# Kernel tuning notes

Measured on AMD Instinct MI355X. Metric: run time of the kernel, lower is better.

## Reference

```python
import jax, jax.numpy as jnp
import numpy as np

N_NODES = 20000
N_EDGES = 640000
IN_DIM = 128
HID = 128
OUT_DIM = 3
N_GRAPHS = 32


def setup_inputs() -> dict:
    key = jax.random.key(0)
    ks = jax.random.split(key, 12)
    x = jax.random.normal(ks[0], (N_NODES, IN_DIM), dtype=jnp.float32)
    edge_index = jax.random.randint(ks[1], (2, N_EDGES), 0, N_NODES, dtype=jnp.int64)
    batch = jnp.sort(jax.random.randint(ks[2], (N_NODES,), 0, N_GRAPHS, dtype=jnp.int64))
    batch = batch.at[0].set(0).at[-1].set(N_GRAPHS - 1)
    s = 0.05
    W_gcn = jax.random.normal(ks[3], (IN_DIM, HID), jnp.float32) * s
    b_gcn = jnp.zeros((HID,), jnp.float32)
    W_sage_l = jax.random.normal(ks[4], (HID, HID), jnp.float32) * s  # neighbor branch
    W_sage_r = jax.random.normal(ks[5], (HID, HID), jnp.float32) * s  # root branch
    b_sage = jnp.zeros((HID,), jnp.float32)
    W_fc1 = jax.random.normal(ks[6], (HID, HID), jnp.float32) * s
    b_fc1 = jnp.zeros((HID,), jnp.float32)
    W_fc2 = jax.random.normal(ks[7], (HID, OUT_DIM), jnp.float32) * s
    b_fc2 = jnp.zeros((OUT_DIM,), jnp.float32)
    return {
        'x': x, 'edge_index': edge_index, 'batch': batch,
        'W_gcn': W_gcn, 'b_gcn': b_gcn,
        'W_sage_l': W_sage_l, 'W_sage_r': W_sage_r, 'b_sage': b_sage,
        'W_fc1': W_fc1, 'b_fc1': b_fc1, 'W_fc2': W_fc2, 'b_fc2': b_fc2,
    }


def reference(x, edge_index, batch, W_gcn, b_gcn, W_sage_l, W_sage_r, b_sage,
              W_fc1, b_fc1, W_fc2, b_fc2):
    n = x.shape[0]
    row, col = edge_index[0], edge_index[1]  # source -> target

    # ---- GCNConv: symmetric-normalized aggregation with self-loops ----
    h = x @ W_gcn  # [N, H]
    loops = jnp.arange(n, dtype=row.dtype)
    row_sl = jnp.concatenate([row, loops])
    col_sl = jnp.concatenate([col, loops])
    deg = jax.ops.segment_sum(jnp.ones_like(col_sl, dtype=h.dtype), col_sl,
                              num_segments=n)
    dinv = jnp.where(deg > 0, jax.lax.rsqrt(deg), 0.0)
    norm = dinv[row_sl] * dinv[col_sl]  # [E+N]
    h_gcn = jax.ops.segment_sum(h[row_sl] * norm[:, None], col_sl,
                                num_segments=n) + b_gcn
    h_gcn = jax.nn.relu(h_gcn)

    # ---- SAGEConv (mean aggregator) ----
    cnt = jax.ops.segment_sum(jnp.ones_like(col, dtype=h_gcn.dtype), col,
                              num_segments=n)
    neigh = jax.ops.segment_sum(h_gcn[row], col, num_segments=n)
    neigh = neigh / jnp.maximum(cnt, 1.0)[:, None]
    h_sage = neigh @ W_sage_l + h_gcn @ W_sage_r + b_sage
    h_sage = jax.nn.relu(h_sage)

    # ---- global_add_pool (num_graphs = 32 < 50) ----
    pooled = jax.ops.segment_sum(h_sage, batch, num_segments=N_GRAPHS)  # [G, H]

    # ---- MLP head ----
    out = jax.nn.relu(pooled @ W_fc1 + b_fc1) @ W_fc2 + b_fc2  # [G, 3]
    return out
```

## Files before the change

kernel.cpp:

```cpp
#include <hip/hip_runtime.h>

#define N_NODES 20000
#define N_EDGES 640000
#define HID 128
#define N_GRAPHS 32

__global__ __launch_bounds__(256) void hist_k(const int* __restrict__ col,
                                              int* __restrict__ cnt) {
    int e = blockIdx.x * blockDim.x + threadIdx.x;
    if (e < N_EDGES) {
        int c = col[e];
        if ((unsigned)c < N_NODES) atomicAdd(&cnt[c], 1);
    }
}

__global__ __launch_bounds__(1024) void scan_k(const int* __restrict__ cnt,
                                               int* __restrict__ offs,
                                               int* __restrict__ cursor,
                                               float* __restrict__ dinv) {
    __shared__ int sums[1024];
    const int t = threadIdx.x;
    const int CHUNK = 20;
    int base = t * CHUNK;
    int s = 0;
    for (int j = 0; j < CHUNK; ++j) {
        int i = base + j;
        if (i < N_NODES) s += cnt[i];
    }
    sums[t] = s;
    __syncthreads();
    for (int off = 1; off < 1024; off <<= 1) {
        int v = sums[t];
        int add = (t >= off) ? sums[t - off] : 0;
        __syncthreads();
        sums[t] = v + add;
        __syncthreads();
    }
    int run = (t > 0) ? sums[t - 1] : 0;
    for (int j = 0; j < CHUNK; ++j) {
        int i = base + j;
        if (i < N_NODES) {
            offs[i] = run;
            cursor[i] = run;
            int c = cnt[i];
            run += c;
            dinv[i] = rsqrtf((float)(c + 1));
        }
    }
    if (t == 1023) offs[N_NODES] = run;
}

__global__ __launch_bounds__(256) void fill_k(const int* __restrict__ row,
                                              const int* __restrict__ col,
                                              int* __restrict__ cursor,
                                              int* __restrict__ csr_src,
                                              float* __restrict__ csr_norm,
                                              const float* __restrict__ dinv) {
    int e = blockIdx.x * blockDim.x + threadIdx.x;
    if (e < N_EDGES) {
        int c = col[e];
        int r = row[e];
        if ((unsigned)c < N_NODES && (unsigned)r < N_NODES) {
            int p = atomicAdd(&cursor[c], 1);
            csr_src[p] = r;
            csr_norm[p] = dinv[r];
        }
    }
}

__global__ __launch_bounds__(256) void gemm128_k(const float* __restrict__ X,
                                                 const float* __restrict__ W,
                                                 float* __restrict__ Y,
                                                 int nrows) {
    __shared__ float ws[128 * 128];
    __shared__ float xs[32 * 128];
    const int t = threadIdx.x;
    for (int i = t; i < 4096; i += 256)
        ((float4*)ws)[i] = ((const float4*)W)[i];
    const int rg = t >> 5;
    const int c4 = (t & 31) * 4;
    const int ntiles = (nrows + 31) / 32;
    for (int tile = blockIdx.x; tile < ntiles; tile += gridDim.x) {
        const int row0 = tile * 32;
        __syncthreads();
#pragma unroll
        for (int i = 0; i < 4; ++i) {
            int idx = t + i * 256;
            int rr = row0 + (idx >> 5);
            float4 v = (rr < nrows) ? ((const float4*)X)[(size_t)rr * 32 + (idx & 31)]
                                    : make_float4(0.f, 0.f, 0.f, 0.f);
            ((float4*)xs)[idx] = v;
        }
        __syncthreads();
        float4 acc[4];
        acc[0] = acc[1] = acc[2] = acc[3] = make_float4(0.f, 0.f, 0.f, 0.f);
#pragma unroll 4
        for (int k = 0; k < 128; k += 2) {
            float4 w0 = *(const float4*)&ws[(k + 0) * 128 + c4];
            float4 w1 = *(const float4*)&ws[(k + 1) * 128 + c4];
#pragma unroll
            for (int i = 0; i < 4; ++i) {
                float2 xv = *(const float2*)&xs[(rg * 4 + i) * 128 + k];
                acc[i].x = fmaf(xv.x, w0.x, fmaf(xv.y, w1.x, acc[i].x));
                acc[i].y = fmaf(xv.x, w0.y, fmaf(xv.y, w1.y, acc[i].y));
                acc[i].z = fmaf(xv.x, w0.z, fmaf(xv.y, w1.z, acc[i].z));
                acc[i].w = fmaf(xv.x, w0.w, fmaf(xv.y, w1.w, acc[i].w));
            }
        }
#pragma unroll
        for (int i = 0; i < 4; ++i) {
            int rr = row0 + rg * 4 + i;
            if (rr < nrows) *(float4*)&Y[(size_t)rr * 128 + c4] = acc[i];
        }
    }
}

__global__ __launch_bounds__(256) void gcn_agg_k(const float* __restrict__ h,
                                                 const int* __restrict__ offs,
                                                 const int* __restrict__ src,
                                                 const float* __restrict__ nrm,
                                                 const float* __restrict__ dinv,
                                                 const float* __restrict__ bias,
                                                 float* __restrict__ out) {
    const int wave = threadIdx.x >> 6;
    const int lane = threadIdx.x & 63;
    const int half = lane >> 5;
    const int node = (blockIdx.x * 4 + wave) * 2 + half;
    const int c4 = (lane & 31) * 4;
    const int nd = (node < N_NODES) ? node : (N_NODES - 1);
    const float dc = dinv[nd];
    float4 hv = *(const float4*)&h[(size_t)nd * 128 + c4];
    float4 acc = make_float4(dc * hv.x, dc * hv.y, dc * hv.z, dc * hv.w);
    const int beg = offs[nd];
    const int deg = offs[nd + 1] - beg;
    const int mdeg = max(deg, __shfl(deg, lane ^ 32));
    for (int j = 0; j < mdeg; j += 4) {
        int i0 = (j + 0 < deg) ? beg + j + 0 : 0;
        int i1 = (j + 1 < deg) ? beg + j + 1 : 0;
        int i2 = (j + 2 < deg) ? beg + j + 2 : 0;
        int i3 = (j + 3 < deg) ? beg + j + 3 : 0;
        float w0 = (j + 0 < deg) ? nrm[i0] : 0.f;
        float w1 = (j + 1 < deg) ? nrm[i1] : 0.f;
        float w2 = (j + 2 < deg) ? nrm[i2] : 0.f;
        float w3 = (j + 3 < deg) ? nrm[i3] : 0.f;
        int s0 = src[i0], s1 = src[i1], s2 = src[i2], s3 = src[i3];
        float4 v0 = *(const float4*)&h[(size_t)s0 * 128 + c4];
        float4 v1 = *(const float4*)&h[(size_t)s1 * 128 + c4];
        float4 v2 = *(const float4*)&h[(size_t)s2 * 128 + c4];
        float4 v3 = *(const float4*)&h[(size_t)s3 * 128 + c4];
        acc.x = fmaf(w0, v0.x, fmaf(w1, v1.x, fmaf(w2, v2.x, fmaf(w3, v3.x, acc.x))));
        acc.y = fmaf(w0, v0.y, fmaf(w1, v1.y, fmaf(w2, v2.y, fmaf(w3, v3.y, acc.y))));
        acc.z = fmaf(w0, v0.z, fmaf(w1, v1.z, fmaf(w2, v2.z, fmaf(w3, v3.z, acc.z))));
        acc.w = fmaf(w0, v0.w, fmaf(w1, v1.w, fmaf(w2, v2.w, fmaf(w3, v3.w, acc.w))));
    }
    float4 b = *(const float4*)&bias[c4];
    float4 o;
    o.x = fmaxf(fmaf(dc, acc.x, b.x), 0.f);
    o.y = fmaxf(fmaf(dc, acc.y, b.y), 0.f);
    o.z = fmaxf(fmaf(dc, acc.z, b.z), 0.f);
    o.w = fmaxf(fmaf(dc, acc.w, b.w), 0.f);
    if (node < N_NODES) *(float4*)&out[(size_t)node * 128 + c4] = o;
}

__global__ __launch_bounds__(256) void sage_agg_k(const float* __restrict__ hg,
                                                  const int* __restrict__ offs,
                                                  const int* __restrict__ src,
                                                  float* __restrict__ out) {
    const int wave = threadIdx.x >> 6;
    const int lane = threadIdx.x & 63;
    const int half = lane >> 5;
    const int node = (blockIdx.x * 4 + wave) * 2 + half;
    const int c4 = (lane & 31) * 4;
    const int nd = (node < N_NODES) ? node : (N_NODES - 1);
    float4 acc = make_float4(0.f, 0.f, 0.f, 0.f);
    const int beg = offs[nd];
    const int deg = offs[nd + 1] - beg;
    const int mdeg = max(deg, __shfl(deg, lane ^ 32));
    for (int j = 0; j < mdeg; j += 4) {
        int i0 = (j + 0 < deg) ? beg + j + 0 : 0;
        int i1 = (j + 1 < deg) ? beg + j + 1 : 0;
        int i2 = (j + 2 < deg) ? beg + j + 2 : 0;
        int i3 = (j + 3 < deg) ? beg + j + 3 : 0;
        float w0 = (j + 0 < deg) ? 1.f : 0.f;
        float w1 = (j + 1 < deg) ? 1.f : 0.f;
        float w2 = (j + 2 < deg) ? 1.f : 0.f;
        float w3 = (j + 3 < deg) ? 1.f : 0.f;
        int s0 = src[i0], s1 = src[i1], s2 = src[i2], s3 = src[i3];
        float4 v0 = *(const float4*)&hg[(size_t)s0 * 128 + c4];
        float4 v1 = *(const float4*)&hg[(size_t)s1 * 128 + c4];
        float4 v2 = *(const float4*)&hg[(size_t)s2 * 128 + c4];
        float4 v3 = *(const float4*)&hg[(size_t)s3 * 128 + c4];
        acc.x = fmaf(w0, v0.x, fmaf(w1, v1.x, fmaf(w2, v2.x, fmaf(w3, v3.x, acc.x))));
        acc.y = fmaf(w0, v0.y, fmaf(w1, v1.y, fmaf(w2, v2.y, fmaf(w3, v3.y, acc.y))));
        acc.z = fmaf(w0, v0.z, fmaf(w1, v1.z, fmaf(w2, v2.z, fmaf(w3, v3.z, acc.z))));
        acc.w = fmaf(w0, v0.w, fmaf(w1, v1.w, fmaf(w2, v2.w, fmaf(w3, v3.w, acc.w))));
    }
    float inv = 1.0f / (float)max(deg, 1);
    float4 o;
    o.x = acc.x * inv;
    o.y = acc.y * inv;
    o.z = acc.z * inv;
    o.w = acc.w * inv;
    if (node < N_NODES) *(float4*)&out[(size_t)node * 128 + c4] = o;
}

__global__ __launch_bounds__(256) void combine_k(const float* __restrict__ An,
                                                 const float* __restrict__ Bh,
                                                 const float* __restrict__ Wl,
                                                 const float* __restrict__ Wr,
                                                 const float* __restrict__ bias,
                                                 float* __restrict__ Y) {
    __shared__ float ws[128 * 128];
    __shared__ float xs[32 * 128];
    const int t = threadIdx.x;
    const int rg = t >> 5;
    const int c4 = (t & 31) * 4;
    const int ntiles = (N_NODES + 31) / 32;
    for (int tile = blockIdx.x; tile < ntiles; tile += gridDim.x) {
        const int row0 = tile * 32;
        float4 acc[4];
        {
            float4 b = *(const float4*)&bias[c4];
            acc[0] = acc[1] = acc[2] = acc[3] = b;
        }
#pragma unroll
        for (int m = 0; m < 2; ++m) {
            const float* Wm = m ? Wr : Wl;
            const float* Xm = m ? Bh : An;
            __syncthreads();
            for (int i = t; i < 4096; i += 256)
                ((float4*)ws)[i] = ((const float4*)Wm)[i];
#pragma unroll
            for (int i = 0; i < 4; ++i) {
                int idx = t + i * 256;
                int rr = row0 + (idx >> 5);
                float4 v = (rr < N_NODES) ? ((const float4*)Xm)[(size_t)rr * 32 + (idx & 31)]
                                          : make_float4(0.f, 0.f, 0.f, 0.f);
                ((float4*)xs)[idx] = v;
            }
            __syncthreads();
#pragma unroll 4
            for (int k = 0; k < 128; k += 2) {
                float4 w0 = *(const float4*)&ws[(k + 0) * 128 + c4];
                float4 w1 = *(const float4*)&ws[(k + 1) * 128 + c4];
#pragma unroll
                for (int i = 0; i < 4; ++i) {
                    float2 xv = *(const float2*)&xs[(rg * 4 + i) * 128 + k];
                    acc[i].x = fmaf(xv.x, w0.x, fmaf(xv.y, w1.x, acc[i].x));
                    acc[i].y = fmaf(xv.x, w0.y, fmaf(xv.y, w1.y, acc[i].y));
                    acc[i].z = fmaf(xv.x, w0.z, fmaf(xv.y, w1.z, acc[i].z));
                    acc[i].w = fmaf(xv.x, w0.w, fmaf(xv.y, w1.w, acc[i].w));
                }
            }
        }
#pragma unroll
        for (int i = 0; i < 4; ++i) {
            int rr = row0 + rg * 4 + i;
            if (rr < N_NODES) {
                float4 o = acc[i];
                o.x = fmaxf(o.x, 0.f);
                o.y = fmaxf(o.y, 0.f);
                o.z = fmaxf(o.z, 0.f);
                o.w = fmaxf(o.w, 0.f);
                *(float4*)&Y[(size_t)rr * 128 + c4] = o;
            }
        }
    }
}

#define POOL_ROWS 64
__global__ __launch_bounds__(256) void pool_k(const float* __restrict__ H,
                                              const int* __restrict__ batch,
                                              float* __restrict__ pooled) {
    const int r0 = blockIdx.x * POOL_ROWS;
    const int t = threadIdx.x;
    const int d = t & 127, half = t >> 7;
    const int rend = min(r0 + POOL_ROWS, N_NODES);
    int i = r0 + half;
    if (i >= rend) return;
    int cur = batch[i];
    float acc = 0.f;
    for (; i < rend; i += 2) {
        int g = batch[i];
        if (g != cur) {
            atomicAdd(&pooled[cur * 128 + d], acc);
            acc = 0.f;
            cur = g;
        }
        acc += H[(size_t)i * 128 + d];
    }
    atomicAdd(&pooled[cur * 128 + d], acc);
}

__global__ __launch_bounds__(128) void head_k(const float* __restrict__ pooled,
                                              const float* __restrict__ Wfc1,
                                              const float* __restrict__ bfc1,
                                              const float* __restrict__ Wfc2,
                                              const float* __restrict__ bfc2,
                                              float* __restrict__ out) {
    __shared__ float pl[128];
    __shared__ float tmp[128];
    const int g = blockIdx.x;
    const int t = threadIdx.x;
    pl[t] = pooled[g * 128 + t];
    __syncthreads();
    float a = bfc1[t];
#pragma unroll 8
    for (int k = 0; k < 128; ++k) a = fmaf(pl[k], Wfc1[k * 128 + t], a);
    tmp[t] = fmaxf(a, 0.f);
    __syncthreads();
    if (t < 3) {
        float a2 = bfc2[t];
        for (int k = 0; k < 128; ++k) a2 = fmaf(tmp[k], Wfc2[k * 3 + t], a2);
        out[g * 3 + t] = a2;
    }
}

extern "C" void kernel_launch(void* const* d_in, const int* in_sizes, int n_in,
                              void* d_out, int out_size, void* d_ws, size_t ws_size,
                              hipStream_t stream) {
    const float* x      = (const float*)d_in[0];
    const int*   ei     = (const int*)d_in[1];
    const int*   batch  = (const int*)d_in[2];
    const float* W_gcn  = (const float*)d_in[3];
    const float* b_gcn  = (const float*)d_in[4];
    const float* W_sl   = (const float*)d_in[5];
    const float* W_sr   = (const float*)d_in[6];
    const float* b_sage = (const float*)d_in[7];
    const float* W_fc1  = (const float*)d_in[8];
    const float* b_fc1  = (const float*)d_in[9];
    const float* W_fc2  = (const float*)d_in[10];
    const float* b_fc2  = (const float*)d_in[11];
    float* out = (float*)d_out;

    char* base = (char*)d_ws;
    size_t off = 0;
    auto take = [&](size_t bytes) -> void* {
        void* p = base + off;
        off += (bytes + 255) & ~(size_t)255;
        return p;
    };
    int*   cnt      = (int*)take((size_t)N_NODES * 4);
    int*   offs     = (int*)take((size_t)(N_NODES + 1) * 4);
    int*   cursor   = (int*)take((size_t)N_NODES * 4);
    float* dinv     = (float*)take((size_t)N_NODES * 4);
    int*   csr_src  = (int*)take((size_t)N_EDGES * 4);
    float* csr_norm = (float*)take((size_t)N_EDGES * 4);
    float* bufA     = (float*)take((size_t)N_NODES * HID * 4);
    float* bufB     = (float*)take((size_t)N_NODES * HID * 4);
    float* pooled   = (float*)take((size_t)N_GRAPHS * HID * 4);

    const int* row = ei;
    const int* col = ei + N_EDGES;

    hipMemsetAsync(cnt, 0, (size_t)N_NODES * 4, stream);
    hipMemsetAsync(pooled, 0, (size_t)N_GRAPHS * HID * 4, stream);

    hist_k<<<(N_EDGES + 255) / 256, 256, 0, stream>>>(col, cnt);
    scan_k<<<1, 1024, 0, stream>>>(cnt, offs, cursor, dinv);
    fill_k<<<(N_EDGES + 255) / 256, 256, 0, stream>>>(row, col, cursor, csr_src, csr_norm, dinv);

    const int ntiles = (N_NODES + 31) / 32;
    const int agg_blocks = (N_NODES + 7) / 8;
    gemm128_k<<<ntiles, 256, 0, stream>>>(x, W_gcn, bufA, N_NODES);
    gcn_agg_k<<<agg_blocks, 256, 0, stream>>>(bufA, offs, csr_src, csr_norm,
                                              dinv, b_gcn, bufB);
    sage_agg_k<<<agg_blocks, 256, 0, stream>>>(bufB, offs, csr_src, bufA);
    combine_k<<<ntiles, 256, 0, stream>>>(bufA, bufB, W_sl, W_sr, b_sage, bufA);
    pool_k<<<(N_NODES + POOL_ROWS - 1) / POOL_ROWS, 256, 0, stream>>>(bufA, batch, pooled);
    head_k<<<N_GRAPHS, 128, 0, stream>>>(pooled, W_fc1, b_fc1, W_fc2, b_fc2, out);
}
```

Baseline: 351.1 us.

## Split single-block prefix scan into multi-block reduce-then-scan kernels

Replaces the single 1024-thread block scan over node degrees with two kernels: one computes per-block sums with wavefront shuffles, the second does a block-local scan and adds a serially computed block prefix. The aim is to spread the scan across many CUs instead of one, so the strided serial chunk loops and their uncoalesced loads go away. It adds an extra kernel launch and a serial loop over up to 79 block sums per block.

```diff
diff --git a/kernel.cpp b/kernel.cpp
--- a/kernel.cpp
+++ b/kernel.cpp
@@ -4,6 +4,9 @@
 #define N_EDGES 640000
 #define HID 128
 #define N_GRAPHS 32
+
+#define SCAN_BLK 256
+#define SCAN_NBLK ((N_NODES + SCAN_BLK - 1) / SCAN_BLK)
 
 __global__ __launch_bounds__(256) void hist_k(const int* __restrict__ col,
                                               int* __restrict__ cnt) {
@@ -14,40 +17,54 @@
     }
 }
 
-__global__ __launch_bounds__(1024) void scan_k(const int* __restrict__ cnt,
-                                               int* __restrict__ offs,
-                                               int* __restrict__ cursor,
-                                               float* __restrict__ dinv) {
-    __shared__ int sums[1024];
-    const int t = threadIdx.x;
-    const int CHUNK = 20;
-    int base = t * CHUNK;
-    int s = 0;
-    for (int j = 0; j < CHUNK; ++j) {
-        int i = base + j;
-        if (i < N_NODES) s += cnt[i];
-    }
-    sums[t] = s;
+__global__ __launch_bounds__(SCAN_BLK) void scanA_k(const int* __restrict__ cnt,
+                                                    int* __restrict__ blkSum) {
+    __shared__ int wsum[SCAN_BLK / 64];
+    const int b = blockIdx.x, t = threadIdx.x;
+    const int i = b * SCAN_BLK + t;
+    int v = (i < N_NODES) ? cnt[i] : 0;
+#pragma unroll
+    for (int o = 1; o < 64; o <<= 1) v += __shfl_xor(v, o);
+    if ((t & 63) == 0) wsum[t >> 6] = v;
     __syncthreads();
-    for (int off = 1; off < 1024; off <<= 1) {
-        int v = sums[t];
-        int add = (t >= off) ? sums[t - off] : 0;
+    if (t == 0) {
+        int s = 0;
+#pragma unroll
+        for (int w = 0; w < SCAN_BLK / 64; ++w) s += wsum[w];
+        blkSum[b] = s;
+    }
+}
+
+__global__ __launch_bounds__(SCAN_BLK) void scanB_k(const int* __restrict__ cnt,
+                                                    const int* __restrict__ blkSum,
+                                                    int* __restrict__ offs,
+                                                    int* __restrict__ cursor,
+                                                    float* __restrict__ dinv) {
+    __shared__ int sm[SCAN_BLK];
+    __shared__ int base_s;
+    const int b = blockIdx.x, t = threadIdx.x;
+    const int i = b * SCAN_BLK + t;
+    const int v = (i < N_NODES) ? cnt[i] : 0;
+    sm[t] = v;
+    if (t == 0) {
+        int s = 0;
+        for (int k = 0; k < b; ++k) s += blkSum[k];
+        base_s = s;
+    }
+    __syncthreads();
+    for (int o = 1; o < SCAN_BLK; o <<= 1) {
+        int add = (t >= o) ? sm[t - o] : 0;
         __syncthreads();
-        sums[t] = v + add;
+        sm[t] += add;
         __syncthreads();
     }
-    int run = (t > 0) ? sums[t - 1] : 0;
-    for (int j = 0; j < CHUNK; ++j) {
-        int i = base + j;
-        if (i < N_NODES) {
-            offs[i] = run;
-            cursor[i] = run;
-            int c = cnt[i];
-            run += c;
-            dinv[i] = rsqrtf((float)(c + 1));
-        }
-    }
-    if (t == 1023) offs[N_NODES] = run;
+    if (i < N_NODES) {
+        int excl = base_s + ((t > 0) ? sm[t - 1] : 0);
+        offs[i] = excl;
+        cursor[i] = excl;
+        dinv[i] = rsqrtf((float)(v + 1));
+        if (i == N_NODES - 1) offs[N_NODES] = excl + v;
+    }
 }
 
 __global__ __launch_bounds__(256) void fill_k(const int* __restrict__ row,
@@ -344,6 +361,7 @@
     int*   offs     = (int*)take((size_t)(N_NODES + 1) * 4);
     int*   cursor   = (int*)take((size_t)N_NODES * 4);
     float* dinv     = (float*)take((size_t)N_NODES * 4);
+    int*   blkSum   = (int*)take((size_t)SCAN_NBLK * 4);
     int*   csr_src  = (int*)take((size_t)N_EDGES * 4);
     float* csr_norm = (float*)take((size_t)N_EDGES * 4);
     float* bufA     = (float*)take((size_t)N_NODES * HID * 4);
@@ -357,7 +375,8 @@
     hipMemsetAsync(pooled, 0, (size_t)N_GRAPHS * HID * 4, stream);
 
     hist_k<<<(N_EDGES + 255) / 256, 256, 0, stream>>>(col, cnt);
-    scan_k<<<1, 1024, 0, stream>>>(cnt, offs, cursor, dinv);
+    scanA_k<<<SCAN_NBLK, SCAN_BLK, 0, stream>>>(cnt, blkSum);
+    scanB_k<<<SCAN_NBLK, SCAN_BLK, 0, stream>>>(cnt, blkSum, offs, cursor, dinv);
     fill_k<<<(N_EDGES + 255) / 256, 256, 0, stream>>>(row, col, cursor, csr_src, csr_norm, dinv);
 
     const int ntiles = (N_NODES + 31) / 32;
```

Result: faster. 314.9 us (-10.3%).
